# Performance work log

Hardware: AMD Instinct MI355X
Metric: run time of the kernel (lower is better)

Reference implementation:

```python
import jax, jax.numpy as jnp
import numpy as np

N = 50000
E = 800000
NUM_IDS = 2048
IN_CH = 16
HID = 32
HEADS = 4
EMB = 8
GAT_IN = EMB + (IN_CH - 1)  # 23
NEG_SLOPE = 0.2


def gat_layer(x, src, dst, W, a_src, a_dst, b):
    """PyG-style GATConv (self-loops already appended to src/dst).
    x: [N, Fin]; W: [Fin, H*C]; a_src/a_dst: [H, C]; b: [H*C].
    Returns [N, H*C] (heads concatenated)."""
    H, C = a_src.shape
    h = (x @ W).reshape(-1, H, C)                      # [N,H,C]
    alpha_s = jnp.sum(h * a_src, axis=-1)              # [N,H]
    alpha_d = jnp.sum(h * a_dst, axis=-1)              # [N,H]
    e = jax.nn.leaky_relu(alpha_s[src] + alpha_d[dst], NEG_SLOPE)  # [E',H]
    # segment softmax over destination neighborhoods
    m = jax.ops.segment_max(e, dst, num_segments=N)    # [N,H]
    ex = jnp.exp(e - m[dst])
    denom = jax.ops.segment_sum(ex, dst, num_segments=N)
    alpha = ex / (denom[dst] + 1e-16)                  # [E',H]
    msg = h[src] * alpha[:, :, None]                   # [E',H,C]
    out = jax.ops.segment_sum(msg, dst, num_segments=N)  # [N,H,C]
    return out.reshape(-1, H * C) + b


def setup_inputs() -> dict:
    key = jax.random.key(0)
    ks = jax.random.split(key, 20)
    node_ids = jax.random.randint(ks[0], (N,), 0, NUM_IDS, dtype=jnp.int32)
    node_feats = jax.random.normal(ks[1], (N, IN_CH - 1), dtype=jnp.float32)
    src = jax.random.randint(ks[2], (E,), 0, N, dtype=jnp.int32)
    off = jax.random.randint(ks[3], (E,), 1, N, dtype=jnp.int32)
    dst = (src + off) % N  # guarantee no pre-existing self-loops
    edge_index = jnp.stack([src, dst]).astype(jnp.int32)
    batch = jnp.zeros((N,), dtype=jnp.int32)

    def w(k, shape):
        return jax.random.normal(k, shape, dtype=jnp.float32) * 0.1

    emb = w(ks[4], (NUM_IDS, EMB))
    # enc1: GAT_IN -> HID, heads=HEADS
    W1, a1s, a1d, b1 = w(ks[5], (GAT_IN, HEADS * HID)), w(ks[6], (HEADS, HID)), w(ks[7], (HEADS, HID)), jnp.zeros((HEADS * HID,), jnp.float32)
    # enc2: HID*HEADS -> HID, heads=1
    W2, a2s, a2d, b2 = w(ks[8], (HEADS * HID, HID)), w(ks[9], (1, HID)), w(ks[10], (1, HID)), jnp.zeros((HID,), jnp.float32)
    # dec1: HID -> HID, heads=HEADS
    W3, a3s, a3d, b3 = w(ks[11], (HID, HEADS * HID)), w(ks[12], (HEADS, HID)), w(ks[13], (HEADS, HID)), jnp.zeros((HEADS * HID,), jnp.float32)
    # dec2: HID*HEADS -> IN_CH, heads=1
    W4, a4s, a4d, b4 = w(ks[14], (HEADS * HID, IN_CH)), w(ks[15], (1, IN_CH)), w(ks[16], (1, IN_CH)), jnp.zeros((IN_CH,), jnp.float32)
    return {"node_ids": node_ids, "node_feats": node_feats, "edge_index": edge_index,
            "batch": batch, "emb": emb,
            "W1": W1, "a1s": a1s, "a1d": a1d, "b1": b1,
            "W2": W2, "a2s": a2s, "a2d": a2d, "b2": b2,
            "W3": W3, "a3s": a3s, "a3d": a3d, "b3": b3,
            "W4": W4, "a4s": a4s, "a4d": a4d, "b4": b4}


def reference(node_ids, node_feats, edge_index, batch, emb,
              W1, a1s, a1d, b1, W2, a2s, a2d, b2,
              W3, a3s, a3d, b3, W4, a4s, a4d, b4):
    # PyG GATConv adds self-loops by default
    loop = jnp.arange(N, dtype=edge_index.dtype)
    src = jnp.concatenate([edge_index[0], loop])
    dst = jnp.concatenate([edge_index[1], loop])
    x = jnp.concatenate([emb[node_ids], node_feats], axis=1)  # [N, GAT_IN]
    x = jax.nn.relu(gat_layer(x, src, dst, W1, a1s, a1d, b1))
    x = jax.nn.relu(gat_layer(x, src, dst, W2, a2s, a2d, b2))
    x = jax.nn.relu(gat_layer(x, src, dst, W3, a3s, a3d, b3))
    x = jax.nn.sigmoid(gat_layer(x, src, dst, W4, a4s, a4d, b4))
    return x
```

## Files before the change

kernel.cpp:

```cpp
#include <hip/hip_runtime.h>
#include <hip/hip_bf16.h>

typedef __hip_bfloat16 bf16;
typedef float f32x2 __attribute__((ext_vector_type(2)));

#define NEG_SLOPE 0.2f
#define DCAP 128

__device__ __forceinline__ float b2f(bf16 v) { return __bfloat162float(v); }
__device__ __forceinline__ float lrelu(float x) { return x >= 0.f ? x : NEG_SLOPE * x; }
__device__ __forceinline__ float2 bf2x(unsigned pv) {
    float2 r;
    r.x = __uint_as_float(pv << 16);
    r.y = __uint_as_float(pv & 0xffff0000u);
    return r;
}
__device__ __forceinline__ f32x2 bfp(unsigned pv) {
    f32x2 r;
    r.x = __uint_as_float(pv << 16);
    r.y = __uint_as_float(pv & 0xffff0000u);
    return r;
}
__device__ __forceinline__ void fma8p(f32x2* acc, float w, uint4 pv) {
    f32x2 wv = {w, w};
    acc[0] += wv * bfp(pv.x);
    acc[1] += wv * bfp(pv.y);
    acc[2] += wv * bfp(pv.z);
    acc[3] += wv * bfp(pv.w);
}

static inline int cdiv(int a, int b) { return (a + b - 1) / b; }

__global__ void fill_sentinel(float* __restrict__ y, int n) {
    int t = blockIdx.x * 256 + threadIdx.x;
    if (t < n) y[t] = 2.0f;
}

__global__ __launch_bounds__(256) void init_and_t1(
    int* __restrict__ cursor, int IB,
    const int* __restrict__ ids, const float* __restrict__ feats,
    const float* __restrict__ emb, const float* __restrict__ W1,
    const float* __restrict__ a1s, const float* __restrict__ a1d,
    bf16* __restrict__ h_out, float* __restrict__ as_out, float* __restrict__ ad_out, int N) {
    if ((int)blockIdx.x < IB) {
        int i = blockIdx.x * 256 + threadIdx.x;
        if (i < N) cursor[i] = i * DCAP;
        return;
    }
    constexpr int FIN = 23, FINP = 27, HC = 128;
    __shared__ float xs[2 * FINP];
    const int node0 = (blockIdx.x - IB) * 2;
    const int tid = threadIdx.x;
    if (tid < 2 * FIN) {
        int ln = tid / FIN, f = tid - ln * FIN;
        int i = node0 + ln;
        float v = 0.f;
        if (i < N) v = (f < 8) ? emb[ids[i] * 8 + f] : feats[i * 15 + (f - 8)];
        xs[ln * FINP + f] = v;
    }
    __syncthreads();
    const int ln = tid >> 7, j = tid & 127;
    const int i = node0 + ln;
    if (i >= N) return;
    float acc = 0.f;
#pragma unroll
    for (int f = 0; f < FIN; ++f) acc += xs[ln * FINP + f] * W1[f * HC + j];
    h_out[(size_t)i * HC + j] = __float2bfloat16(acc);
    float s = acc * a1s[j];
    float d = acc * a1d[j];
#pragma unroll
    for (int off = 16; off > 0; off >>= 1) {
        s += __shfl_down(s, off, 32);
        d += __shfl_down(d, off, 32);
    }
    if ((j & 31) == 0) {
        as_out[i * 4 + j / 32] = s;
        ad_out[i * 4 + j / 32] = d;
    }
}

template <typename EIDX>
__global__ void fill_direct(const int* __restrict__ src, const int* __restrict__ dst,
                            int* __restrict__ cursor, EIDX* __restrict__ elsrc, int E) {
    int t = blockIdx.x * 256 + threadIdx.x;
    if (t >= E) return;
    int d = dst[t];
    int slot = atomicAdd(&cursor[d], 1);
    if (slot < d * DCAP + DCAP) elsrc[slot] = (EIDX)src[t];
}

template <int H, int C, int HN, int CN, bool FINAL, typename EIDX>
__global__ __launch_bounds__(256) void gat_tf(
    const int* __restrict__ cursor, const EIDX* __restrict__ elsrc,
    const bf16* __restrict__ hIn, const float* __restrict__ asIn,
    const float* __restrict__ adIn, const float* __restrict__ bias,
    const float* __restrict__ Wn, const float* __restrict__ anS,
    const float* __restrict__ anD, bf16* __restrict__ hOut,
    float* __restrict__ asOut, float* __restrict__ adOut,
    float* __restrict__ yout, int N) {
    constexpr int HC = H * C;
    constexpr int HCN = HN * CN;
    constexpr int LPR = HC / 8;
    constexpr int EPI = 64 / LPR;
    constexpr int HCP = HC + 4;
    __shared__ int src_s[256];
    __shared__ float w_s[256 * H];
    __shared__ float xs[FINAL ? 1 : 4 * HCP];
    const int wvi = threadIdx.x >> 6;
    const int lane = threadIdx.x & 63;
    const int d = blockIdx.x * 4 + wvi;
    if (d >= N) return;
    const int grp = lane / LPR;
    const int lin = lane - grp * LPR;
    const int ch0 = 8 * lin;
    const int h0 = ch0 / C;

    {
        const int row = d * DCAP;
        const int s_pre = (int)elsrc[row + lane];
        const int end = min(cursor[d], row + DCAP);
        float ad_d[H], c[H], den_p[H];
        if constexpr (H == 4) {
            float4 adv = *(const float4*)(adIn + d * 4);
            float4 asv = *(const float4*)(asIn + d * 4);
            ad_d[0] = adv.x; ad_d[1] = adv.y; ad_d[2] = adv.z; ad_d[3] = adv.w;
            c[0] = lrelu(asv.x + adv.x);
            c[1] = lrelu(asv.y + adv.y);
            c[2] = lrelu(asv.z + adv.z);
            c[3] = lrelu(asv.w + adv.w);
            den_p[0] = den_p[1] = den_p[2] = den_p[3] = 0.f;
        } else {
#pragma unroll
            for (int h = 0; h < H; ++h) {
                ad_d[h] = adIn[d * H + h];
                c[h] = lrelu(asIn[d * H + h] + ad_d[h]);
                den_p[h] = 0.f;
            }
        }
        f32x2 acc[4];
#pragma unroll
        for (int q = 0; q < 4; ++q) acc[q] = (f32x2){0.f, 0.f};
        if (grp == 0) {
            uint4 pv = *(const uint4*)(hIn + (size_t)d * HC + ch0);
            acc[0] = bfp(pv.x);
            acc[1] = bfp(pv.y);
            acc[2] = bfp(pv.z);
            acc[3] = bfp(pv.w);
        }
        for (int base = row; base < end; base += 64) {
            int e = base + lane;
            int s = (base == row) ? s_pre : ((e < end) ? (int)elsrc[e] : -1);
            if (e >= end) s = -1;
            if constexpr (H == 4) {
                float4 w4 = {0.f, 0.f, 0.f, 0.f};
                if (s >= 0) {
                    float4 av = *(const float4*)(asIn + s * 4);
                    w4.x = __expf(lrelu(av.x + ad_d[0]) - c[0]);
                    w4.y = __expf(lrelu(av.y + ad_d[1]) - c[1]);
                    w4.z = __expf(lrelu(av.z + ad_d[2]) - c[2]);
                    w4.w = __expf(lrelu(av.w + ad_d[3]) - c[3]);
                    den_p[0] += w4.x;
                    den_p[1] += w4.y;
                    den_p[2] += w4.z;
                    den_p[3] += w4.w;
                }
                *(float4*)&w_s[(wvi * 64 + lane) * 4] = w4;
            } else {
                float w0 = 0.f;
                if (s >= 0) {
                    w0 = __expf(lrelu(asIn[s] + ad_d[0]) - c[0]);
                    den_p[0] += w0;
                }
                w_s[wvi * 64 + lane] = w0;
            }
            src_s[wvi * 64 + lane] = (s >= 0) ? s : 0;
            int nv = min(64, end - base);
#pragma unroll 4
            for (int k0 = 0; k0 < nv; k0 += EPI) {
                int k = k0 + grp;
                if (k < nv) {
                    int sk = src_s[wvi * 64 + k];
                    float w = w_s[(wvi * 64 + k) * H + h0];
                    uint4 pv = *(const uint4*)(hIn + (size_t)sk * HC + ch0);
                    fma8p(acc, w, pv);
                }
            }
        }
#pragma unroll
        for (int h = 0; h < H; ++h) {
            float v = den_p[h];
#pragma unroll
            for (int o = 32; o > 0; o >>= 1) v += __shfl_xor(v, o, 64);
            den_p[h] = v + 1.0f;
        }
#pragma unroll
        for (int o = LPR; o < 64; o <<= 1) {
#pragma unroll
            for (int q = 0; q < 4; ++q) {
                acc[q].x += __shfl_xor(acc[q].x, o, 64);
                acc[q].y += __shfl_xor(acc[q].y, o, 64);
            }
        }
        if (grp == 0) {
            float inv = 1.f / (den_p[h0] + 1e-16f);
            float v[8];
#pragma unroll
            for (int q = 0; q < 4; ++q) {
                v[2 * q] = acc[q].x * inv + bias[ch0 + 2 * q];
                v[2 * q + 1] = acc[q].y * inv + bias[ch0 + 2 * q + 1];
            }
            if constexpr (FINAL) {
                float4 o0, o1;
                o0.x = 1.f / (1.f + __expf(-v[0]));
                o0.y = 1.f / (1.f + __expf(-v[1]));
                o0.z = 1.f / (1.f + __expf(-v[2]));
                o0.w = 1.f / (1.f + __expf(-v[3]));
                o1.x = 1.f / (1.f + __expf(-v[4]));
                o1.y = 1.f / (1.f + __expf(-v[5]));
                o1.z = 1.f / (1.f + __expf(-v[6]));
                o1.w = 1.f / (1.f + __expf(-v[7]));
                *(float4*)(yout + (size_t)d * HC + ch0) = o0;
                *(float4*)(yout + (size_t)d * HC + ch0 + 4) = o1;
            } else {
#pragma unroll
                for (int r = 0; r < 8; ++r)
                    xs[wvi * HCP + ch0 + r] = v[r] > 0.f ? v[r] : 0.f;
            }
        }
    }

    if constexpr (!FINAL) {
        __builtin_amdgcn_wave_barrier();
        const float* xrow = xs + wvi * HCP;
        if constexpr (HCN == 128) {
            int j0 = lane, j1 = lane + 64;
            float a0 = 0.f, a1 = 0.f;
#pragma unroll
            for (int f = 0; f < HC; f += 4) {
                float4 xv = *(const float4*)&xrow[f];
                a0 += xv.x * Wn[(f + 0) * HCN + j0] + xv.y * Wn[(f + 1) * HCN + j0] +
                      xv.z * Wn[(f + 2) * HCN + j0] + xv.w * Wn[(f + 3) * HCN + j0];
                a1 += xv.x * Wn[(f + 0) * HCN + j1] + xv.y * Wn[(f + 1) * HCN + j1] +
                      xv.z * Wn[(f + 2) * HCN + j1] + xv.w * Wn[(f + 3) * HCN + j1];
            }
            hOut[(size_t)d * HCN + j0] = __float2bfloat16(a0);
            hOut[(size_t)d * HCN + j1] = __float2bfloat16(a1);
            float s0 = a0 * anS[j0], d0 = a0 * anD[j0];
            float s1 = a1 * anS[j1], d1 = a1 * anD[j1];
#pragma unroll
            for (int o = 16; o > 0; o >>= 1) {
                s0 += __shfl_down(s0, o, 32);
                d0 += __shfl_down(d0, o, 32);
                s1 += __shfl_down(s1, o, 32);
                d1 += __shfl_down(d1, o, 32);
            }
            if ((lane & 31) == 0) {
                int hh = lane >> 5;
                asOut[d * 4 + hh] = s0;
                adOut[d * 4 + hh] = d0;
                asOut[d * 4 + 2 + hh] = s1;
                adOut[d * 4 + 2 + hh] = d1;
            }
        } else {
            constexpr int LPO = 64 / HCN;
            constexpr int FSEG = HC / LPO;
            const int j = lane % HCN;
            const int seg = lane / HCN;
            const int f0 = seg * FSEG;
            float a = 0.f;
#pragma unroll
            for (int f = 0; f < FSEG; f += 4) {
                float4 xv = *(const float4*)&xrow[f0 + f];
                a += xv.x * Wn[(f0 + f + 0) * HCN + j] + xv.y * Wn[(f0 + f + 1) * HCN + j] +
                     xv.z * Wn[(f0 + f + 2) * HCN + j] + xv.w * Wn[(f0 + f + 3) * HCN + j];
            }
#pragma unroll
            for (int o = HCN; o < 64; o <<= 1) a += __shfl_xor(a, o, 64);
            if (seg == 0) hOut[(size_t)d * HCN + j] = __float2bfloat16(a);
            float sv = a * anS[j];
            float dv = a * anD[j];
#pragma unroll
            for (int o = HCN / 2; o > 0; o >>= 1) {
                sv += __shfl_down(sv, o, HCN);
                dv += __shfl_down(dv, o, HCN);
            }
            if (lane == 0) {
                asOut[d] = sv;
                adOut[d] = dv;
            }
        }
    }
}

template <typename EIDX>
static void run_layers(const int* cursor, const EIDX* elsrc, bf16* hA, bf16* hB,
                       float* asA, float* adA, float* asB, float* adB, float* y,
                       void* const* d_in, int N, hipStream_t stream) {
    const float* b1 = (const float*)d_in[8];
    const float* W2 = (const float*)d_in[9];
    const float* a2s = (const float*)d_in[10];
    const float* a2d = (const float*)d_in[11];
    const float* b2 = (const float*)d_in[12];
    const float* W3 = (const float*)d_in[13];
    const float* a3s = (const float*)d_in[14];
    const float* a3d = (const float*)d_in[15];
    const float* b3 = (const float*)d_in[16];
    const float* W4 = (const float*)d_in[17];
    const float* a4s = (const float*)d_in[18];
    const float* a4d = (const float*)d_in[19];
    const float* b4 = (const float*)d_in[20];
    const int g = cdiv(N, 4);
    gat_tf<4, 32, 1, 32, false, EIDX><<<g, 256, 0, stream>>>(
        cursor, elsrc, hA, asA, adA, b1, W2, a2s, a2d, hB, asB, adB, y, N);
    gat_tf<1, 32, 4, 32, false, EIDX><<<g, 256, 0, stream>>>(
        cursor, elsrc, hB, asB, adB, b2, W3, a3s, a3d, hA, asA, adA, y, N);
    gat_tf<4, 32, 1, 16, false, EIDX><<<g, 256, 0, stream>>>(
        cursor, elsrc, hA, asA, adA, b3, W4, a4s, a4d, hB, asB, adB, y, N);
    gat_tf<1, 16, 1, 1, true, EIDX><<<g, 256, 0, stream>>>(
        cursor, elsrc, hB, asB, adB, b4, W4, a4s, a4d, hA, asA, adA, y, N);
}

extern "C" void kernel_launch(void* const* d_in, const int* in_sizes, int n_in,
                              void* d_out, int out_size, void* d_ws, size_t ws_size,
                              hipStream_t stream) {
    const int N = in_sizes[0];
    const int E = in_sizes[2] / 2;
    const int* node_ids = (const int*)d_in[0];
    const float* feats = (const float*)d_in[1];
    const int* srcI = (const int*)d_in[2];
    const int* dstI = srcI + E;
    const float* emb = (const float*)d_in[4];
    const float* W1 = (const float*)d_in[5];
    const float* a1s = (const float*)d_in[6];
    const float* a1d = (const float*)d_in[7];
    float* y = (float*)d_out;

    float* asA = (float*)d_ws;
    float* adA = asA + (size_t)N * 4;
    float* asB = adA + (size_t)N * 4;
    float* adB = asB + (size_t)N * 4;
    bf16* hA = (bf16*)(adB + (size_t)N * 4);
    bf16* hB = hA + (size_t)N * 128;
    int* cursor = (int*)(hB + (size_t)N * 128);
    int* elsrc = cursor + N;

    const bool u16 = (N <= 65536);
    size_t elsz = (size_t)N * DCAP * (u16 ? 2 : 4);
    size_t need = (size_t)N * 4 * 4 * 4 + (size_t)N * 128 * 2 * 2 + (size_t)N * 4 + elsz;
    if (ws_size < need) {
        fill_sentinel<<<cdiv(out_size, 256), 256, 0, stream>>>(y, out_size);
        return;
    }

    const int IB = cdiv(N, 256);
    init_and_t1<<<IB + cdiv(N, 2), 256, 0, stream>>>(cursor, IB, node_ids, feats, emb,
                                                     W1, a1s, a1d, hA, asA, adA, N);
    if (u16) {
        ushort* el16 = (ushort*)elsrc;
        fill_direct<ushort><<<cdiv(E, 256), 256, 0, stream>>>(srcI, dstI, cursor, el16, E);
        run_layers<ushort>(cursor, el16, hA, hB, asA, adA, asB, adB, y, d_in, N, stream);
    } else {
        fill_direct<int><<<cdiv(E, 256), 256, 0, stream>>>(srcI, dstI, cursor, elsrc, E);
        run_layers<int>(cursor, elsrc, hA, hB, asA, adA, asB, adB, y, d_in, N, stream);
    }
}
```

Baseline: 338.9 us.

## Use persistent grid-stride kernels with next-node prefetch and paired-column transform

Converts the init, fill and GAT layer kernels into persistent grid-stride loops capped at 2048 blocks. In the layer kernel, each wave prefetches the next destination node's cursor, first edge indices, self features and attention scalars while it processes the current node. The per-node dense transform is also unified so that each lane computes two adjacent output columns with float2 weight loads and packed bf16 stores. The aim is to cut block launch overhead and hide per-node load latency, at the cost of more registers and possibly lower occupancy or weaker load balance.

```diff
diff --git a/kernel.cpp b/kernel.cpp
--- a/kernel.cpp
+++ b/kernel.cpp
@@ -7,14 +7,7 @@
 #define NEG_SLOPE 0.2f
 #define DCAP 128
 
-__device__ __forceinline__ float b2f(bf16 v) { return __bfloat162float(v); }
 __device__ __forceinline__ float lrelu(float x) { return x >= 0.f ? x : NEG_SLOPE * x; }
-__device__ __forceinline__ float2 bf2x(unsigned pv) {
-    float2 r;
-    r.x = __uint_as_float(pv << 16);
-    r.y = __uint_as_float(pv & 0xffff0000u);
-    return r;
-}
 __device__ __forceinline__ f32x2 bfp(unsigned pv) {
     f32x2 r;
     r.x = __uint_as_float(pv << 16);
@@ -28,8 +21,13 @@
     acc[2] += wv * bfp(pv.z);
     acc[3] += wv * bfp(pv.w);
 }
+__device__ __forceinline__ ushort bfbits(float x) {
+    bf16 b = __float2bfloat16(x);
+    return *reinterpret_cast<ushort*>(&b);
+}
 
 static inline int cdiv(int a, int b) { return (a + b - 1) / b; }
+__host__ __device__ static inline int imin(int a, int b) { return a < b ? a : b; }
 
 __global__ void fill_sentinel(float* __restrict__ y, int n) {
     int t = blockIdx.x * 256 + threadIdx.x;
@@ -42,51 +40,59 @@
     const float* __restrict__ emb, const float* __restrict__ W1,
     const float* __restrict__ a1s, const float* __restrict__ a1d,
     bf16* __restrict__ h_out, float* __restrict__ as_out, float* __restrict__ ad_out, int N) {
-    if ((int)blockIdx.x < IB) {
-        int i = blockIdx.x * 256 + threadIdx.x;
-        if (i < N) cursor[i] = i * DCAP;
-        return;
-    }
     constexpr int FIN = 23, FINP = 27, HC = 128;
     __shared__ float xs[2 * FINP];
-    const int node0 = (blockIdx.x - IB) * 2;
+    const int VB = IB + (N + 1) / 2;
     const int tid = threadIdx.x;
-    if (tid < 2 * FIN) {
-        int ln = tid / FIN, f = tid - ln * FIN;
-        int i = node0 + ln;
-        float v = 0.f;
-        if (i < N) v = (f < 8) ? emb[ids[i] * 8 + f] : feats[i * 15 + (f - 8)];
-        xs[ln * FINP + f] = v;
-    }
-    __syncthreads();
-    const int ln = tid >> 7, j = tid & 127;
-    const int i = node0 + ln;
-    if (i >= N) return;
-    float acc = 0.f;
-#pragma unroll
-    for (int f = 0; f < FIN; ++f) acc += xs[ln * FINP + f] * W1[f * HC + j];
-    h_out[(size_t)i * HC + j] = __float2bfloat16(acc);
-    float s = acc * a1s[j];
-    float d = acc * a1d[j];
-#pragma unroll
-    for (int off = 16; off > 0; off >>= 1) {
-        s += __shfl_down(s, off, 32);
-        d += __shfl_down(d, off, 32);
-    }
-    if ((j & 31) == 0) {
-        as_out[i * 4 + j / 32] = s;
-        ad_out[i * 4 + j / 32] = d;
+    for (int vb = blockIdx.x; vb < VB; vb += gridDim.x) {
+        if (vb < IB) {
+            int i = vb * 256 + tid;
+            if (i < N) cursor[i] = i * DCAP;
+            continue;
+        }
+        const int node0 = (vb - IB) * 2;
+        if (tid < 2 * FIN) {
+            int ln = tid / FIN, f = tid - ln * FIN;
+            int i = node0 + ln;
+            float v = 0.f;
+            if (i < N) v = (f < 8) ? emb[ids[i] * 8 + f] : feats[i * 15 + (f - 8)];
+            xs[ln * FINP + f] = v;
+        }
+        __syncthreads();
+        const int ln = tid >> 7, j = tid & 127;
+        const int i = node0 + ln;
+        if (i < N) {
+            float acc = 0.f;
+#pragma unroll
+            for (int f = 0; f < FIN; ++f) acc += xs[ln * FINP + f] * W1[f * HC + j];
+            h_out[(size_t)i * HC + j] = __float2bfloat16(acc);
+            float s = acc * a1s[j];
+            float d = acc * a1d[j];
+#pragma unroll
+            for (int off = 16; off > 0; off >>= 1) {
+                s += __shfl_down(s, off, 32);
+                d += __shfl_down(d, off, 32);
+            }
+            if ((j & 31) == 0) {
+                as_out[i * 4 + j / 32] = s;
+                ad_out[i * 4 + j / 32] = d;
+            }
+        }
+        __syncthreads();
     }
 }
 
 template <typename EIDX>
-__global__ void fill_direct(const int* __restrict__ src, const int* __restrict__ dst,
-                            int* __restrict__ cursor, EIDX* __restrict__ elsrc, int E) {
-    int t = blockIdx.x * 256 + threadIdx.x;
-    if (t >= E) return;
-    int d = dst[t];
-    int slot = atomicAdd(&cursor[d], 1);
-    if (slot < d * DCAP + DCAP) elsrc[slot] = (EIDX)src[t];
+__global__ __launch_bounds__(256) void fill_direct(const int* __restrict__ src,
+                                                   const int* __restrict__ dst,
+                                                   int* __restrict__ cursor,
+                                                   EIDX* __restrict__ elsrc, int E) {
+    const int stride = gridDim.x * 256;
+    for (int t = blockIdx.x * 256 + threadIdx.x; t < E; t += stride) {
+        int d = dst[t];
+        int slot = atomicAdd(&cursor[d], 1);
+        if (slot < d * DCAP + DCAP) elsrc[slot] = (EIDX)src[t];
+    }
 }
 
 template <int H, int C, int HN, int CN, bool FINAL, typename EIDX>
@@ -108,44 +114,61 @@
     __shared__ float xs[FINAL ? 1 : 4 * HCP];
     const int wvi = threadIdx.x >> 6;
     const int lane = threadIdx.x & 63;
-    const int d = blockIdx.x * 4 + wvi;
+    const int stride4 = gridDim.x * 4;
+    int d = blockIdx.x * 4 + wvi;
     if (d >= N) return;
     const int grp = lane / LPR;
     const int lin = lane - grp * LPR;
     const int ch0 = 8 * lin;
     const int h0 = ch0 / C;
 
-    {
-        const int row = d * DCAP;
-        const int s_pre = (int)elsrc[row + lane];
-        const int end = min(cursor[d], row + DCAP);
+    int cur_n, spre_n;
+    uint4 hself_n;
+    float4 adv_n, asv_n;
+    float ad1_n, as1_n;
+    auto pf = [&](int dd) {
+        cur_n = cursor[dd];
+        spre_n = (int)elsrc[(size_t)dd * DCAP + lane];
+        hself_n = *(const uint4*)(hIn + (size_t)dd * HC + ch0);
+        if constexpr (H == 4) {
+            adv_n = *(const float4*)(adIn + dd * 4);
+            asv_n = *(const float4*)(asIn + dd * 4);
+        } else {
+            ad1_n = adIn[dd];
+            as1_n = asIn[dd];
+        }
+    };
+    pf(d);
+    for (;;) {
+        const int cur = cur_n;
+        const int s_pre = spre_n;
+        const uint4 hself = hself_n;
         float ad_d[H], c[H], den_p[H];
         if constexpr (H == 4) {
-            float4 adv = *(const float4*)(adIn + d * 4);
-            float4 asv = *(const float4*)(asIn + d * 4);
-            ad_d[0] = adv.x; ad_d[1] = adv.y; ad_d[2] = adv.z; ad_d[3] = adv.w;
-            c[0] = lrelu(asv.x + adv.x);
-            c[1] = lrelu(asv.y + adv.y);
-            c[2] = lrelu(asv.z + adv.z);
-            c[3] = lrelu(asv.w + adv.w);
+            ad_d[0] = adv_n.x; ad_d[1] = adv_n.y; ad_d[2] = adv_n.z; ad_d[3] = adv_n.w;
+            c[0] = lrelu(asv_n.x + adv_n.x);
+            c[1] = lrelu(asv_n.y + adv_n.y);
+            c[2] = lrelu(asv_n.z + adv_n.z);
+            c[3] = lrelu(asv_n.w + adv_n.w);
             den_p[0] = den_p[1] = den_p[2] = den_p[3] = 0.f;
         } else {
-#pragma unroll
-            for (int h = 0; h < H; ++h) {
-                ad_d[h] = adIn[d * H + h];
-                c[h] = lrelu(asIn[d * H + h] + ad_d[h]);
-                den_p[h] = 0.f;
-            }
-        }
+            ad_d[0] = ad1_n;
+            c[0] = lrelu(as1_n + ad1_n);
+            den_p[0] = 0.f;
+        }
+        const int dn = d + stride4;
+        if (dn < N) pf(dn);
+
+        const int row = d * DCAP;
+        const int end = imin(cur, row + DCAP);
         f32x2 acc[4];
 #pragma unroll
         for (int q = 0; q < 4; ++q) acc[q] = (f32x2){0.f, 0.f};
         if (grp == 0) {
-            uint4 pv = *(const uint4*)(hIn + (size_t)d * HC + ch0);
-            acc[0] = bfp(pv.x);
-            acc[1] = bfp(pv.y);
-            acc[2] = bfp(pv.z);
-            acc[3] = bfp(pv.w);
+            acc[0] = bfp(hself.x);
+            acc[1] = bfp(hself.y);
+            acc[2] = bfp(hself.z);
+            acc[3] = bfp(hself.w);
         }
         for (int base = row; base < end; base += 64) {
             int e = base + lane;
@@ -174,7 +197,7 @@
                 w_s[wvi * 64 + lane] = w0;
             }
             src_s[wvi * 64 + lane] = (s >= 0) ? s : 0;
-            int nv = min(64, end - base);
+            int nv = imin(64, end - base);
 #pragma unroll 4
             for (int k0 = 0; k0 < nv; k0 += EPI) {
                 int k = k0 + grp;
@@ -227,68 +250,54 @@
                     xs[wvi * HCP + ch0 + r] = v[r] > 0.f ? v[r] : 0.f;
             }
         }
-    }
-
-    if constexpr (!FINAL) {
-        __builtin_amdgcn_wave_barrier();
-        const float* xrow = xs + wvi * HCP;
-        if constexpr (HCN == 128) {
-            int j0 = lane, j1 = lane + 64;
+
+        if constexpr (!FINAL) {
+            __builtin_amdgcn_wave_barrier();
+            const float* xrow = xs + wvi * HCP;
+            constexpr int PJ = HCN / 2;
+            constexpr int SEG = 64 / PJ;
+            constexpr int FSEG = HC / SEG;
+            constexpr int PPH = CN / 2;
+            const int jp = lane % PJ;
+            const int seg = lane / PJ;
+            const int f0 = seg * FSEG;
             float a0 = 0.f, a1 = 0.f;
-#pragma unroll
-            for (int f = 0; f < HC; f += 4) {
-                float4 xv = *(const float4*)&xrow[f];
-                a0 += xv.x * Wn[(f + 0) * HCN + j0] + xv.y * Wn[(f + 1) * HCN + j0] +
-                      xv.z * Wn[(f + 2) * HCN + j0] + xv.w * Wn[(f + 3) * HCN + j0];
-                a1 += xv.x * Wn[(f + 0) * HCN + j1] + xv.y * Wn[(f + 1) * HCN + j1] +
-                      xv.z * Wn[(f + 2) * HCN + j1] + xv.w * Wn[(f + 3) * HCN + j1];
-            }
-            hOut[(size_t)d * HCN + j0] = __float2bfloat16(a0);
-            hOut[(size_t)d * HCN + j1] = __float2bfloat16(a1);
-            float s0 = a0 * anS[j0], d0 = a0 * anD[j0];
-            float s1 = a1 * anS[j1], d1 = a1 * anD[j1];
-#pragma unroll
-            for (int o = 16; o > 0; o >>= 1) {
-                s0 += __shfl_down(s0, o, 32);
-                d0 += __shfl_down(d0, o, 32);
-                s1 += __shfl_down(s1, o, 32);
-                d1 += __shfl_down(d1, o, 32);
-            }
-            if ((lane & 31) == 0) {
-                int hh = lane >> 5;
-                asOut[d * 4 + hh] = s0;
-                adOut[d * 4 + hh] = d0;
-                asOut[d * 4 + 2 + hh] = s1;
-                adOut[d * 4 + 2 + hh] = d1;
-            }
-        } else {
-            constexpr int LPO = 64 / HCN;
-            constexpr int FSEG = HC / LPO;
-            const int j = lane % HCN;
-            const int seg = lane / HCN;
-            const int f0 = seg * FSEG;
-            float a = 0.f;
 #pragma unroll
             for (int f = 0; f < FSEG; f += 4) {
                 float4 xv = *(const float4*)&xrow[f0 + f];
-                a += xv.x * Wn[(f0 + f + 0) * HCN + j] + xv.y * Wn[(f0 + f + 1) * HCN + j] +
-                     xv.z * Wn[(f0 + f + 2) * HCN + j] + xv.w * Wn[(f0 + f + 3) * HCN + j];
-            }
-#pragma unroll
-            for (int o = HCN; o < 64; o <<= 1) a += __shfl_xor(a, o, 64);
-            if (seg == 0) hOut[(size_t)d * HCN + j] = __float2bfloat16(a);
-            float sv = a * anS[j];
-            float dv = a * anD[j];
-#pragma unroll
-            for (int o = HCN / 2; o > 0; o >>= 1) {
-                sv += __shfl_down(sv, o, HCN);
-                dv += __shfl_down(dv, o, HCN);
-            }
-            if (lane == 0) {
-                asOut[d] = sv;
-                adOut[d] = dv;
-            }
-        }
+                float2 w0 = *(const float2*)&Wn[(f0 + f + 0) * HCN + 2 * jp];
+                float2 w1 = *(const float2*)&Wn[(f0 + f + 1) * HCN + 2 * jp];
+                float2 w2 = *(const float2*)&Wn[(f0 + f + 2) * HCN + 2 * jp];
+                float2 w3 = *(const float2*)&Wn[(f0 + f + 3) * HCN + 2 * jp];
+                a0 += xv.x * w0.x + xv.y * w1.x + xv.z * w2.x + xv.w * w3.x;
+                a1 += xv.x * w0.y + xv.y * w1.y + xv.z * w2.y + xv.w * w3.y;
+            }
+#pragma unroll
+            for (int o = PJ; o < 64; o <<= 1) {
+                a0 += __shfl_xor(a0, o, 64);
+                a1 += __shfl_xor(a1, o, 64);
+            }
+            if (seg == 0) {
+                ushort2 st;
+                st.x = bfbits(a0);
+                st.y = bfbits(a1);
+                *(ushort2*)(hOut + (size_t)d * HCN + 2 * jp) = st;
+            }
+            float sv = a0 * anS[2 * jp] + a1 * anS[2 * jp + 1];
+            float dv = a0 * anD[2 * jp] + a1 * anD[2 * jp + 1];
+#pragma unroll
+            for (int o = PPH / 2; o > 0; o >>= 1) {
+                sv += __shfl_down(sv, o, PPH);
+                dv += __shfl_down(dv, o, PPH);
+            }
+            if (seg == 0 && (jp % PPH) == 0) {
+                asOut[d * HN + jp / PPH] = sv;
+                adOut[d * HN + jp / PPH] = dv;
+            }
+        }
+
+        if (dn >= N) break;
+        d = dn;
     }
 }
 
@@ -309,7 +318,7 @@
     const float* a4s = (const float*)d_in[18];
     const float* a4d = (const float*)d_in[19];
     const float* b4 = (const float*)d_in[20];
-    const int g = cdiv(N, 4);
+    const int g = imin(2048, cdiv(N, 4));
     gat_tf<4, 32, 1, 32, false, EIDX><<<g, 256, 0, stream>>>(
         cursor, elsrc, hA, asA, adA, b1, W2, a2s, a2d, hB, asB, adB, y, N);
     gat_tf<1, 32, 4, 32, false, EIDX><<<g, 256, 0, stream>>>(
@@ -353,14 +362,17 @@
     }
 
     const int IB = cdiv(N, 256);
-    init_and_t1<<<IB + cdiv(N, 2), 256, 0, stream>>>(cursor, IB, node_ids, feats, emb,
-                                                     W1, a1s, a1d, hA, asA, adA, N);
+    const int VB = IB + cdiv(N, 2);
+    init_and_t1<<<imin(2048, VB), 256, 0, stream>>>(cursor, IB, node_ids, feats, emb,
+                                                    W1, a1s, a1d, hA, asA, adA, N);
     if (u16) {
         ushort* el16 = (ushort*)elsrc;
-        fill_direct<ushort><<<cdiv(E, 256), 256, 0, stream>>>(srcI, dstI, cursor, el16, E);
+        fill_direct<ushort><<<imin(2048, cdiv(E, 256)), 256, 0, stream>>>(srcI, dstI,
+                                                                          cursor, el16, E);
         run_layers<ushort>(cursor, el16, hA, hB, asA, adA, asB, adB, y, d_in, N, stream);
     } else {
-        fill_direct<int><<<cdiv(E, 256), 256, 0, stream>>>(srcI, dstI, cursor, elsrc, E);
+        fill_direct<int><<<imin(2048, cdiv(E, 256)), 256, 0, stream>>>(srcI, dstI,
+                                                                       cursor, elsrc, E);
         run_layers<int>(cursor, elsrc, hA, hB, asA, adA, asB, adB, y, d_in, N, stream);
     }
 }
```

After: 410.7 us. +21.2%, slower.

## Use persistent grid-stride GAT layers with paired-column packed projection epilogue

Applied to the files above, without the earlier changes.

Caps the grid at 2048 blocks and has each wave loop over destination nodes grid-stride, with launch bounds requesting 8 blocks per CU. The per-node projection epilogue is unified: each lane computes two adjacent output columns with packed f32x2 FMAs and float2 weight loads, stores packed bf16 pairs, and does a narrower attention-logit reduction. The change aims to cut block launch overhead and epilogue instruction count. The tighter register bound risks spills, and fewer blocks may hurt load balance across the skewed per-node degrees.

```diff
diff --git a/kernel.cpp b/kernel.cpp
--- a/kernel.cpp
+++ b/kernel.cpp
@@ -7,14 +7,7 @@
 #define NEG_SLOPE 0.2f
 #define DCAP 128
 
-__device__ __forceinline__ float b2f(bf16 v) { return __bfloat162float(v); }
-__device__ __forceinline__ float lrelu(float x) { return x >= 0.f ? x : NEG_SLOPE * x; }
-__device__ __forceinline__ float2 bf2x(unsigned pv) {
-    float2 r;
-    r.x = __uint_as_float(pv << 16);
-    r.y = __uint_as_float(pv & 0xffff0000u);
-    return r;
-}
+__device__ __forceinline__ float lrelu(float x) { return fmaxf(x, NEG_SLOPE * x); }
 __device__ __forceinline__ f32x2 bfp(unsigned pv) {
     f32x2 r;
     r.x = __uint_as_float(pv << 16);
@@ -28,8 +21,13 @@
     acc[2] += wv * bfp(pv.z);
     acc[3] += wv * bfp(pv.w);
 }
+__device__ __forceinline__ ushort bfbits(float x) {
+    bf16 b = __float2bfloat16(x);
+    return *reinterpret_cast<ushort*>(&b);
+}
 
 static inline int cdiv(int a, int b) { return (a + b - 1) / b; }
+__host__ __device__ static inline int imin(int a, int b) { return a < b ? a : b; }
 
 __global__ void fill_sentinel(float* __restrict__ y, int n) {
     int t = blockIdx.x * 256 + threadIdx.x;
@@ -90,7 +88,7 @@
 }
 
 template <int H, int C, int HN, int CN, bool FINAL, typename EIDX>
-__global__ __launch_bounds__(256) void gat_tf(
+__global__ __launch_bounds__(256, 8) void gat_tf(
     const int* __restrict__ cursor, const EIDX* __restrict__ elsrc,
     const bf16* __restrict__ hIn, const float* __restrict__ asIn,
     const float* __restrict__ adIn, const float* __restrict__ bias,
@@ -108,17 +106,16 @@
     __shared__ float xs[FINAL ? 1 : 4 * HCP];
     const int wvi = threadIdx.x >> 6;
     const int lane = threadIdx.x & 63;
-    const int d = blockIdx.x * 4 + wvi;
-    if (d >= N) return;
+    const int step = gridDim.x * 4;
     const int grp = lane / LPR;
     const int lin = lane - grp * LPR;
     const int ch0 = 8 * lin;
     const int h0 = ch0 / C;
 
-    {
+    for (int d = blockIdx.x * 4 + wvi; d < N; d += step) {
         const int row = d * DCAP;
         const int s_pre = (int)elsrc[row + lane];
-        const int end = min(cursor[d], row + DCAP);
+        const int end = imin(cursor[d], row + DCAP);
         float ad_d[H], c[H], den_p[H];
         if constexpr (H == 4) {
             float4 adv = *(const float4*)(adIn + d * 4);
@@ -130,12 +127,9 @@
             c[3] = lrelu(asv.w + adv.w);
             den_p[0] = den_p[1] = den_p[2] = den_p[3] = 0.f;
         } else {
-#pragma unroll
-            for (int h = 0; h < H; ++h) {
-                ad_d[h] = adIn[d * H + h];
-                c[h] = lrelu(asIn[d * H + h] + ad_d[h]);
-                den_p[h] = 0.f;
-            }
+            ad_d[0] = adIn[d];
+            c[0] = lrelu(asIn[d] + ad_d[0]);
+            den_p[0] = 0.f;
         }
         f32x2 acc[4];
 #pragma unroll
@@ -174,7 +168,7 @@
                 w_s[wvi * 64 + lane] = w0;
             }
             src_s[wvi * 64 + lane] = (s >= 0) ? s : 0;
-            int nv = min(64, end - base);
+            int nv = imin(64, end - base);
 #pragma unroll 4
             for (int k0 = 0; k0 < nv; k0 += EPI) {
                 int k = k0 + grp;
@@ -227,66 +221,53 @@
                     xs[wvi * HCP + ch0 + r] = v[r] > 0.f ? v[r] : 0.f;
             }
         }
-    }
-
-    if constexpr (!FINAL) {
-        __builtin_amdgcn_wave_barrier();
-        const float* xrow = xs + wvi * HCP;
-        if constexpr (HCN == 128) {
-            int j0 = lane, j1 = lane + 64;
-            float a0 = 0.f, a1 = 0.f;
-#pragma unroll
-            for (int f = 0; f < HC; f += 4) {
-                float4 xv = *(const float4*)&xrow[f];
-                a0 += xv.x * Wn[(f + 0) * HCN + j0] + xv.y * Wn[(f + 1) * HCN + j0] +
-                      xv.z * Wn[(f + 2) * HCN + j0] + xv.w * Wn[(f + 3) * HCN + j0];
-                a1 += xv.x * Wn[(f + 0) * HCN + j1] + xv.y * Wn[(f + 1) * HCN + j1] +
-                      xv.z * Wn[(f + 2) * HCN + j1] + xv.w * Wn[(f + 3) * HCN + j1];
-            }
-            hOut[(size_t)d * HCN + j0] = __float2bfloat16(a0);
-            hOut[(size_t)d * HCN + j1] = __float2bfloat16(a1);
-            float s0 = a0 * anS[j0], d0 = a0 * anD[j0];
-            float s1 = a1 * anS[j1], d1 = a1 * anD[j1];
-#pragma unroll
-            for (int o = 16; o > 0; o >>= 1) {
-                s0 += __shfl_down(s0, o, 32);
-                d0 += __shfl_down(d0, o, 32);
-                s1 += __shfl_down(s1, o, 32);
-                d1 += __shfl_down(d1, o, 32);
-            }
-            if ((lane & 31) == 0) {
-                int hh = lane >> 5;
-                asOut[d * 4 + hh] = s0;
-                adOut[d * 4 + hh] = d0;
-                asOut[d * 4 + 2 + hh] = s1;
-                adOut[d * 4 + 2 + hh] = d1;
-            }
-        } else {
-            constexpr int LPO = 64 / HCN;
-            constexpr int FSEG = HC / LPO;
-            const int j = lane % HCN;
-            const int seg = lane / HCN;
+
+        if constexpr (!FINAL) {
+            __builtin_amdgcn_wave_barrier();
+            const float* xrow = xs + wvi * HCP;
+            constexpr int PJ = HCN / 2;
+            constexpr int SEG = 64 / PJ;
+            constexpr int FSEG = HC / SEG;
+            constexpr int PPH = CN / 2;
+            const int jp = lane % PJ;
+            const int seg = lane / PJ;
             const int f0 = seg * FSEG;
-            float a = 0.f;
+            f32x2 ab = {0.f, 0.f};
 #pragma unroll
             for (int f = 0; f < FSEG; f += 4) {
                 float4 xv = *(const float4*)&xrow[f0 + f];
-                a += xv.x * Wn[(f0 + f + 0) * HCN + j] + xv.y * Wn[(f0 + f + 1) * HCN + j] +
-                     xv.z * Wn[(f0 + f + 2) * HCN + j] + xv.w * Wn[(f0 + f + 3) * HCN + j];
-            }
-#pragma unroll
-            for (int o = HCN; o < 64; o <<= 1) a += __shfl_xor(a, o, 64);
-            if (seg == 0) hOut[(size_t)d * HCN + j] = __float2bfloat16(a);
-            float sv = a * anS[j];
-            float dv = a * anD[j];
-#pragma unroll
-            for (int o = HCN / 2; o > 0; o >>= 1) {
-                sv += __shfl_down(sv, o, HCN);
-                dv += __shfl_down(dv, o, HCN);
-            }
-            if (lane == 0) {
-                asOut[d] = sv;
-                adOut[d] = dv;
+                f32x2 w0 = *(const f32x2*)&Wn[(f0 + f + 0) * HCN + 2 * jp];
+                f32x2 w1 = *(const f32x2*)&Wn[(f0 + f + 1) * HCN + 2 * jp];
+                f32x2 w2 = *(const f32x2*)&Wn[(f0 + f + 2) * HCN + 2 * jp];
+                f32x2 w3 = *(const f32x2*)&Wn[(f0 + f + 3) * HCN + 2 * jp];
+                ab += (f32x2){xv.x, xv.x} * w0;
+                ab += (f32x2){xv.y, xv.y} * w1;
+                ab += (f32x2){xv.z, xv.z} * w2;
+                ab += (f32x2){xv.w, xv.w} * w3;
+            }
+#pragma unroll
+            for (int o = PJ; o < 64; o <<= 1) {
+                ab.x += __shfl_xor(ab.x, o, 64);
+                ab.y += __shfl_xor(ab.y, o, 64);
+            }
+            if (seg == 0) {
+                ushort2 st;
+                st.x = bfbits(ab.x);
+                st.y = bfbits(ab.y);
+                *(ushort2*)(hOut + (size_t)d * HCN + 2 * jp) = st;
+            }
+            float2 aS = *(const float2*)&anS[2 * jp];
+            float2 aD = *(const float2*)&anD[2 * jp];
+            float sv = ab.x * aS.x + ab.y * aS.y;
+            float dv = ab.x * aD.x + ab.y * aD.y;
+#pragma unroll
+            for (int o = PPH / 2; o > 0; o >>= 1) {
+                sv += __shfl_down(sv, o, PPH);
+                dv += __shfl_down(dv, o, PPH);
+            }
+            if (seg == 0 && (jp % PPH) == 0) {
+                asOut[d * HN + jp / PPH] = sv;
+                adOut[d * HN + jp / PPH] = dv;
             }
         }
     }
@@ -309,7 +290,7 @@
     const float* a4s = (const float*)d_in[18];
     const float* a4d = (const float*)d_in[19];
     const float* b4 = (const float*)d_in[20];
-    const int g = cdiv(N, 4);
+    const int g = imin(2048, cdiv(N, 4));
     gat_tf<4, 32, 1, 32, false, EIDX><<<g, 256, 0, stream>>>(
         cursor, elsrc, hA, asA, adA, b1, W2, a2s, a2d, hB, asB, adB, y, N);
     gat_tf<1, 32, 4, 32, false, EIDX><<<g, 256, 0, stream>>>(
```

Result: slower. 713.2 us (+110.5%).
